# Optimization experiments

Hardware: AMD Instinct MI355X
Metric: run time of the kernel (lower is better)

Reference implementation:

```python
import jax, jax.numpy as jnp
import numpy as np
from jax import lax

KS = 3            # kernel_size
K = 32            # cluster_num
NB = 32           # num_base_kernels
HID = 64          # mlp_hidden_dim
COUT = 64         # out_channels
MAX_ITER = 20
TOL = 0.005


def _unfold3(x):
    # torch nn.Unfold(k=3, pad=1): output channel order is (c, kh, kw)
    b, c, h, w = x.shape
    xp = jnp.pad(x, ((0, 0), (0, 0), (1, 1), (1, 1)))
    cols = [xp[:, :, i:i + h, j:j + w] for i in range(KS) for j in range(KS)]
    p = jnp.stack(cols, axis=2)  # [B, C, 9, H, W]
    return p.reshape(b, c * KS * KS, h * w).transpose(0, 2, 1)  # [B, HW, C*9]


def _kmeans_single(key, sample):
    # sample: [N, D]. Lloyd iterations with early stop on total center shift.
    n, d = sample.shape
    centers0 = sample[jax.random.permutation(key, n)[:K]]

    def assign(centers):
        d2 = (jnp.sum(sample * sample, 1, keepdims=True)
              - 2.0 * (sample @ centers.T)
              + jnp.sum(centers * centers, 1))
        return jnp.argmin(d2, axis=1)

    def body(carry):
        i, centers, _ = carry
        a = assign(centers)
        oh = jax.nn.one_hot(a, K, dtype=sample.dtype)  # [N, K]
        counts = oh.sum(0)                             # [K]
        sums = oh.T @ sample                           # [K, D]
        new = jnp.where(counts[:, None] > 0,
                        sums / jnp.maximum(counts, 1.0)[:, None],
                        centers)
        shift = jnp.sum(jnp.linalg.norm(new - centers, axis=1))
        return (i + 1, new, shift)

    def cond(carry):
        i, _, shift = carry
        return jnp.logical_and(i < MAX_ITER, shift >= TOL * n)

    init = (jnp.int32(0), centers0, jnp.asarray(jnp.inf, sample.dtype))
    _, centers, _ = lax.while_loop(cond, body, init)
    return assign(centers)


def _kmeans(features):
    keys = jax.random.split(jax.random.key(42), features.shape[0])
    return jax.vmap(_kmeans_single)(keys, features)


def _mlp(x, w1, b1, w2, b2, w3, b3):
    h = jax.nn.relu(x @ w1 + b1)
    h = jax.nn.relu(h @ w2 + b2)
    return h @ w3 + b3


def setup_inputs() -> dict:
    key = jax.random.key(0)
    ks = jax.random.split(key, 16)
    B, C, H, W = 2, 32, 64, 64
    F = C * KS * KS
    fan = 1.0 / np.sqrt(F)
    fanh = 1.0 / np.sqrt(HID)
    return {
        'x': jax.random.normal(ks[0], (B, C, H, W), jnp.float32),
        'base_kernels': jax.random.normal(ks[1], (NB, F, COUT), jnp.float32) * np.sqrt(2.0 / F),
        'kg_w1': jax.random.normal(ks[2], (F, HID), jnp.float32) * fan,
        'kg_b1': jnp.zeros((HID,), jnp.float32),
        'kg_w2': jax.random.normal(ks[3], (HID, HID), jnp.float32) * fanh,
        'kg_b2': jnp.zeros((HID,), jnp.float32),
        'kg_w3': jax.random.normal(ks[4], (HID, NB), jnp.float32) * fanh,
        'kg_b3': jnp.zeros((NB,), jnp.float32),
        'bg_w1': jax.random.normal(ks[5], (F, HID), jnp.float32) * fan,
        'bg_b1': jnp.zeros((HID,), jnp.float32),
        'bg_w2': jax.random.normal(ks[6], (HID, HID), jnp.float32) * fanh,
        'bg_b2': jnp.zeros((HID,), jnp.float32),
        'bg_w3': jax.random.normal(ks[7], (HID, COUT), jnp.float32) * fanh,
        'bg_b3': jnp.zeros((COUT,), jnp.float32),
    }


def reference(x, base_kernels, kg_w1, kg_b1, kg_w2, kg_b2, kg_w3, kg_b3,
              bg_w1, bg_b1, bg_w2, bg_b2, bg_w3, bg_b3):
    B, C, H, W = x.shape
    patches = _unfold3(x)  # [B, P, F] with F = C*9
    P = patches.shape[1]
    # observation features: mean over kernel area per channel
    obs = patches.reshape(B, P, C, KS * KS).mean(-1)  # [B, P, C]
    idx = _kmeans(obs)  # [B, P] int cluster assignments

    # per-cluster centers of the full patch features (scatter-mean)
    oh = jax.nn.one_hot(idx, K, dtype=patches.dtype)          # [B, P, K]
    sums = jnp.einsum('bpk,bpf->bkf', oh, patches)            # [B, K, F]
    counts = jnp.maximum(oh.sum(1), 1.0)                      # [B, K]
    centers = sums / counts[:, :, None]                       # [B, K, F]

    # adaptive kernels = softmax-mixture of base kernels
    attn = jax.nn.softmax(_mlp(centers, kg_w1, kg_b1, kg_w2, kg_b2, kg_w3, kg_b3), axis=-1)  # [B,K,NB]
    kernels = jnp.einsum('bkn,nfc->bkfc', attn, base_kernels)  # [B, K, F, COUT]
    biases = _mlp(centers, bg_w1, bg_b1, bg_w2, bg_b2, bg_w3, bg_b3)  # [B, K, COUT]

    # combine: out[b,p] = patches[b,p] @ kernels[b, idx[b,p]] + biases[b, idx[b,p]]
    bidx = jnp.arange(B)[:, None]
    wtok = kernels[bidx, idx]   # [B, P, F, COUT]
    btok = biases[bidx, idx]    # [B, P, COUT]
    out = jnp.einsum('bpf,bpfc->bpc', patches, wtok) + btok
    out = out.transpose(0, 2, 1).reshape(B, COUT, H, W)
    return (out, idx)
```

## Files before the change

### kernel.cpp

```cpp
#include <hip/hip_runtime.h>
#include <hip/hip_bf16.h>
#include <vector>
#include <algorithm>
#include <utility>
#include <stdint.h>

#define BB 2
#define PP 4096
#define FF 288
#define KK 32
#define NBASE 32
#define HID 64
#define COUT 64
#define NWG_KM 32
#define SUBS 16
#define OUT_ELEMS 524288

#define THREEFRY_PARTITIONABLE 1

typedef unsigned short u16;

#define OFF_IDX    512
#define OFF_ATTN   33280
#define OFF_BIAS   41472
#define OFF_PART   57856
#define OFF_CNTS   320000
#define OFF_CPART  328192
#define OFF_WG     1544704
#define OFF_BAR2   3904000

struct InitIdx { int v[2][32]; };

__device__ __forceinline__ float bf2f(u16 u){
  union { unsigned int i; float f; } cv; cv.i = ((unsigned int)u) << 16; return cv.f;
}
__device__ __forceinline__ u16 f2bf(float f){
  union { float f; unsigned int i; } cv; cv.f = f;
  unsigned int x = cv.i;
  unsigned int r = (x + 0x7FFFu + ((x >> 16) & 1u)) >> 16;
  return (u16)r;
}
__device__ __forceinline__ float u_lo(unsigned int u){
  union { unsigned int i; float f; } cv; cv.i = u << 16; return cv.f;
}
__device__ __forceinline__ float u_hi(unsigned int u){
  union { unsigned int i; float f; } cv; cv.i = u & 0xFFFF0000u; return cv.f;
}

__device__ __forceinline__ void st_agent(float* p, float v){
  __hip_atomic_store(reinterpret_cast<unsigned int*>(p), __float_as_uint(v),
                     __ATOMIC_RELAXED, __HIP_MEMORY_SCOPE_AGENT);
}
__device__ __forceinline__ float ld_agent(const float* p){
  unsigned int u = __hip_atomic_load(reinterpret_cast<const unsigned int*>(p),
                                     __ATOMIC_RELAXED, __HIP_MEMORY_SCOPE_AGENT);
  return __uint_as_float(u);
}
__device__ __forceinline__ void st_slot(int* p, int v){
  __hip_atomic_store(p, v, __ATOMIC_RELAXED, __HIP_MEMORY_SCOPE_AGENT);
}
__device__ __forceinline__ int ld_slot(const int* p){
  return __hip_atomic_load(p, __ATOMIC_RELAXED, __HIP_MEMORY_SCOPE_AGENT);
}

template<bool BF>
__device__ __forceinline__ float ld(const void* p, size_t i){
  if constexpr (BF) { return bf2f(((const u16*)p)[i]); }
  else              { return ((const float*)p)[i]; }
}
template<bool BF>
__device__ __forceinline__ void st(void* p, size_t i, float v){
  if constexpr (BF) { ((u16*)p)[i] = f2bf(v); }
  else              { ((float*)p)[i] = v; }
}

__device__ __forceinline__ bool self_detect(const void* x, int* cntS){
  const int t = threadIdx.x, nb = blockDim.x;
  if (t == 0) *cntS = 0;
  __syncthreads();
  const u16* p = (const u16*)x;
  int bad = 0;
  for (int i = t; i < 1024; i += nb){
    u16 u = p[2*i];
    unsigned e = (u >> 7) & 0xFFu;
    if (e >= 131u) ++bad;
  }
  if (bad) atomicAdd(cntS, bad);
  __syncthreads();
  bool r = (*cntS < 102);
  __syncthreads();
  return r;
}

template<bool BF>
__device__ __forceinline__ float obs_chan(const void* x, size_t bi, int h, int w){
  float s = 0.f;
  #pragma unroll
  for (int dh=-1; dh<=1; ++dh){
    int hh = h + dh;
    #pragma unroll
    for (int dw=-1; dw<=1; ++dw){
      int ww = w + dw;
      float v = 0.f;
      if ((unsigned)hh < 64u && (unsigned)ww < 64u) v = ld<BF>(x, bi + (hh<<6) + ww);
      s += v;
    }
  }
  return s / 9.0f;
}

__device__ __forceinline__ void gbar16(int* slots, int mb, int sub, int epoch){
  asm volatile("s_waitcnt vmcnt(0)" ::: "memory");
  __syncthreads();
  const int t = threadIdx.x;
  if (t == 0) st_slot(&slots[(mb*16 + sub)*16], epoch);
  if (t < 16){
    while (ld_slot(&slots[(mb*16 + t)*16]) < epoch){}
  }
  __atomic_signal_fence(__ATOMIC_SEQ_CST);
  __syncthreads();
}

template<bool BF>
__device__ void kB_body(const void* __restrict__ x,
                        float* __restrict__ part,
                        float* __restrict__ cnts,
                        int* __restrict__ idxg,
                        void* __restrict__ dout,
                        int* __restrict__ slots,
                        const InitIdx& ii,
                        float* obs_st,
                        float* cent,
                        float* cc_s,
                        int*   a_loc,
                        float* sq,
                        float* snorm,
                        float* cntsh,
                        float* acc8,
                        float* cnt8){
  const int t   = threadIdx.x;
  const int wg  = blockIdx.x;
  const int mb  = wg >> 4;
  const int sub = wg & 15;
  const int pg  = sub*256 + t;
  const int d   = t & 31, oct = t >> 5;

  float o[32];
  {
    int h = pg >> 6, w = pg & 63;
    size_t xb = (size_t)mb << 17;
    for (int c=0; c<32; ++c){
      float v = obs_chan<BF>(x, xb + ((size_t)c<<12), h, w);
      o[c] = v; obs_st[t*33 + c] = v;
    }
  }
  if (t < 32){
    int q = ii.v[mb][t];
    int qh = q >> 6, qw = q & 63;
    size_t xq = (size_t)mb << 17;
    for (int c=0; c<32; ++c) cent[t*32 + c] = obs_chan<BF>(x, xq + ((size_t)c<<12), qh, qw);
  }
  __syncthreads();

  float ss = 0.f;
  #pragma unroll
  for (int dd=0; dd<32; ++dd) ss = fmaf(o[dd], o[dd], ss);

  bool act = true;
  int parity = 0;

  for (int it=0; it<20 && act; ++it){
    if (t < 32){
      float s = 0.f;
      #pragma unroll
      for (int dd=0; dd<32; ++dd){ float v = cent[t*32 + dd]; s = fmaf(v,v,s); }
      cc_s[t] = s;
    }
    __syncthreads();
    float best = 3.0e38f; int bk = 0;
    for (int k=0; k<32; k+=4){
      const float4* c0 = (const float4*)&cent[(k  )*32];
      const float4* c1 = (const float4*)&cent[(k+1)*32];
      const float4* c2 = (const float4*)&cent[(k+2)*32];
      const float4* c3 = (const float4*)&cent[(k+3)*32];
      float dt0=0.f, dt1=0.f, dt2=0.f, dt3=0.f;
      #pragma unroll
      for (int q=0; q<8; ++q){
        float4 a0 = c0[q], a1 = c1[q], a2 = c2[q], a3 = c3[q];
        float o0 = o[q*4+0], o1 = o[q*4+1], o2 = o[q*4+2], o3 = o[q*4+3];
        dt0 = fmaf(o0,a0.x,dt0); dt0 = fmaf(o1,a0.y,dt0); dt0 = fmaf(o2,a0.z,dt0); dt0 = fmaf(o3,a0.w,dt0);
        dt1 = fmaf(o0,a1.x,dt1); dt1 = fmaf(o1,a1.y,dt1); dt1 = fmaf(o2,a1.z,dt1); dt1 = fmaf(o3,a1.w,dt1);
        dt2 = fmaf(o0,a2.x,dt2); dt2 = fmaf(o1,a2.y,dt2); dt2 = fmaf(o2,a2.z,dt2); dt2 = fmaf(o3,a2.w,dt2);
        dt3 = fmaf(o0,a3.x,dt3); dt3 = fmaf(o1,a3.y,dt3); dt3 = fmaf(o2,a3.z,dt3); dt3 = fmaf(o3,a3.w,dt3);
      }
      float di0 = (ss - 2.0f*dt0) + cc_s[k];
      float di1 = (ss - 2.0f*dt1) + cc_s[k+1];
      float di2 = (ss - 2.0f*dt2) + cc_s[k+2];
      float di3 = (ss - 2.0f*dt3) + cc_s[k+3];
      if (di0 < best){ best = di0; bk = k; }
      if (di1 < best){ best = di1; bk = k+1; }
      if (di2 < best){ best = di2; bk = k+2; }
      if (di3 < best){ best = di3; bk = k+3; }
    }
    a_loc[t] = bk;
    __syncthreads();
    for (int e=t; e<8*32*33; e+=256) acc8[e] = 0.f;
    cnt8[t] = 0.f;
    __syncthreads();
    {
      const int p0 = oct*32;
      int kcur = a_loc[p0];
      float racc = 0.f; int rl = 0;
      for (int i=0; i<32; ++i){
        int kp = a_loc[p0+i];
        float v = obs_st[(p0+i)*33 + d];
        if (kp != kcur){
          acc8[(oct*32 + kcur)*33 + d] += racc;
          if (d == 0) cnt8[oct*32 + kcur] += (float)rl;
          racc = 0.f; rl = 0; kcur = kp;
        }
        racc += v; ++rl;
      }
      acc8[(oct*32 + kcur)*33 + d] += racc;
      if (d == 0) cnt8[oct*32 + kcur] += (float)rl;
    }
    __syncthreads();
    float* Pg = part + ((size_t)((parity*2 + mb)*SUBS + sub))*1024;
    {
      float r0=0.f, r1=0.f, r2=0.f, r3=0.f;
      #pragma unroll
      for (int o2=0; o2<8; ++o2){
        r0 += acc8[(o2*32 + oct      )*33 + d];
        r1 += acc8[(o2*32 + oct + 8  )*33 + d];
        r2 += acc8[(o2*32 + oct + 16 )*33 + d];
        r3 += acc8[(o2*32 + oct + 24 )*33 + d];
      }
      st_agent(&Pg[(oct     )*32 + d], r0);
      st_agent(&Pg[(oct + 8 )*32 + d], r1);
      st_agent(&Pg[(oct + 16)*32 + d], r2);
      st_agent(&Pg[(oct + 24)*32 + d], r3);
    }
    if (t < 32){
      float c = 0.f;
      #pragma unroll
      for (int o2=0; o2<8; ++o2) c += cnt8[o2*32 + t];
      st_agent(&cnts[((size_t)((parity*2 + mb)*SUBS + sub))*32 + t], c);
    }
    gbar16(slots, mb, sub, it+1);
    {
      const float* Pb = part + (size_t)((parity*2 + mb)*SUBS)*1024;
      const float* Cb = cnts + (size_t)((parity*2 + mb)*SUBS)*32;
      if (t < 32){
        float s = 0.f;
        #pragma unroll
        for (int si=0; si<SUBS; ++si) s += ld_agent(&Cb[si*32 + t]);
        cntsh[t] = s;
      }
      __syncthreads();
      {
        int k = t >> 3, d4 = (t & 7) * 4;
        float vx = 0.f, vy = 0.f, vz = 0.f, vw = 0.f;
        #pragma unroll
        for (int si=0; si<SUBS; ++si){
          const float* pp = &Pb[si*1024 + k*32 + d4];
          float a0 = ld_agent(pp+0);
          float a1 = ld_agent(pp+1);
          float a2 = ld_agent(pp+2);
          float a3 = ld_agent(pp+3);
          vx += a0; vy += a1; vz += a2; vw += a3;
        }
        float cn = cntsh[k];
        float den = fmaxf(cn, 1.f);
        bool pos = cn > 0.f;
        float o0 = cent[k*32 + d4+0], o1 = cent[k*32 + d4+1];
        float o2 = cent[k*32 + d4+2], o3 = cent[k*32 + d4+3];
        float n0 = pos ? (vx / den) : o0;
        float n1 = pos ? (vy / den) : o1;
        float n2 = pos ? (vz / den) : o2;
        float n3 = pos ? (vw / den) : o3;
        float e0 = n0-o0, e1 = n1-o1, e2 = n2-o2, e3 = n3-o3;
        sq[k*32 + d4+0] = e0*e0; sq[k*32 + d4+1] = e1*e1;
        sq[k*32 + d4+2] = e2*e2; sq[k*32 + d4+3] = e3*e3;
        cent[k*32 + d4+0] = n0; cent[k*32 + d4+1] = n1;
        cent[k*32 + d4+2] = n2; cent[k*32 + d4+3] = n3;
      }
      __syncthreads();
      if (t < 32){
        float s = 0.f;
        #pragma unroll
        for (int dd=0; dd<32; ++dd) s += sq[t*32 + dd];
        snorm[t] = sqrtf(s);
      }
      __syncthreads();
      float sh = 0.f;
      for (int k=0;k<32;++k) sh += snorm[k];
      act = ((it+1) < 20) && ((double)sh >= 20.48);
      __syncthreads();
    }
    parity ^= 1;
  }
  if (t == 0) st_slot(&slots[(mb*16 + sub)*16], 0x7FFFFFFF);
  __syncthreads();
  if (t < 32){
    float s = 0.f;
    #pragma unroll
    for (int dd=0; dd<32; ++dd){ float v = cent[t*32 + dd]; s = fmaf(v,v,s); }
    cc_s[t] = s;
  }
  __syncthreads();
  float best = 3.0e38f; int bk = 0;
  for (int k=0; k<32; k+=4){
    const float4* c0 = (const float4*)&cent[(k  )*32];
    const float4* c1 = (const float4*)&cent[(k+1)*32];
    const float4* c2 = (const float4*)&cent[(k+2)*32];
    const float4* c3 = (const float4*)&cent[(k+3)*32];
    float dt0=0.f, dt1=0.f, dt2=0.f, dt3=0.f;
    #pragma unroll
    for (int q=0; q<8; ++q){
      float4 a0 = c0[q], a1 = c1[q], a2 = c2[q], a3 = c3[q];
      float o0 = o[q*4+0], o1 = o[q*4+1], o2 = o[q*4+2], o3 = o[q*4+3];
      dt0 = fmaf(o0,a0.x,dt0); dt0 = fmaf(o1,a0.y,dt0); dt0 = fmaf(o2,a0.z,dt0); dt0 = fmaf(o3,a0.w,dt0);
      dt1 = fmaf(o0,a1.x,dt1); dt1 = fmaf(o1,a1.y,dt1); dt1 = fmaf(o2,a1.z,dt1); dt1 = fmaf(o3,a1.w,dt1);
      dt2 = fmaf(o0,a2.x,dt2); dt2 = fmaf(o1,a2.y,dt2); dt2 = fmaf(o2,a2.z,dt2); dt2 = fmaf(o3,a2.w,dt2);
      dt3 = fmaf(o0,a3.x,dt3); dt3 = fmaf(o1,a3.y,dt3); dt3 = fmaf(o2,a3.z,dt3); dt3 = fmaf(o3,a3.w,dt3);
    }
    float di0 = (ss - 2.0f*dt0) + cc_s[k];
    float di1 = (ss - 2.0f*dt1) + cc_s[k+1];
    float di2 = (ss - 2.0f*dt2) + cc_s[k+2];
    float di3 = (ss - 2.0f*dt3) + cc_s[k+3];
    if (di0 < best){ best = di0; bk = k; }
    if (di1 < best){ best = di1; bk = k+1; }
    if (di2 < best){ best = di2; bk = k+2; }
    if (di3 < best){ best = di3; bk = k+3; }
  }
  idxg[mb*PP + pg] = bk;
  st<BF>(dout, (size_t)OUT_ELEMS + mb*PP + pg, (float)bk);
}

__global__ __launch_bounds__(256) void kB(const void* x, float* part, float* cnts,
                                          int* idxg, void* dout,
                                          int* slots, InitIdx ii){
  __shared__ __align__(16) float obs_st[256*33];
  __shared__ __align__(16) float cent[32*32];
  __shared__ float cc_s[32];
  __shared__ int   a_loc[256];
  __shared__ float sq[32*32];
  __shared__ float snorm[32];
  __shared__ float cntsh[32];
  __shared__ float acc8[8*32*33];
  __shared__ float cnt8[8*32];
  __shared__ int   cntS;
  if (self_detect(x, &cntS))
       kB_body<true >(x, part, cnts, idxg, dout, slots, ii,
                      obs_st, cent, cc_s, a_loc, sq, snorm, cntsh, acc8, cnt8);
  else kB_body<false>(x, part, cnts, idxg, dout, slots, ii,
                      obs_st, cent, cc_s, a_loc, sq, snorm, cntsh, acc8, cnt8);
}

template<bool BF>
__device__ void kC_body(const void* __restrict__ x,
                        const int* __restrict__ idxg,
                        float* __restrict__ cpartJ,
                        float* __restrict__ acc,
                        int* __restrict__ idxsh){
  int wgid = blockIdx.x;
  int cg = wgid / 9, j = wgid % 9;
  int b = cg >> 4, pc = cg & 15;
  int t = threadIdx.x;
  for (int e=t; e<32*33; e+=256) acc[e] = 0.f;
  idxsh[t] = idxg[b*PP + pc*256 + t];
  __syncthreads();

  int dh = j/3 - 1, dw = j%3 - 1;
  int gp = (pc << 8) + t;
  int h = gp >> 6, w = gp & 63;
  int k = idxsh[t];
  int hh = h + dh, ww = w + dw;
  bool ok = ((unsigned)hh < 64u) && ((unsigned)ww < 64u);
  size_t boff = ((size_t)b << 17) + (hh << 6) + ww;

  #pragma unroll 4
  for (int c=0; c<32; ++c){
    float v = ok ? ld<BF>(x, boff + ((size_t)c << 12)) : 0.f;
    atomicAdd(&acc[k*33 + c], v);
  }
  if (j == 0) atomicAdd(&acc[k*33 + 32], 1.0f);
  __syncthreads();
  float* cp = cpartJ + (size_t)wgid*(32*33);
  for (int e=t; e<32*33; e+=256) cp[e] = acc[e];
}

__global__ __launch_bounds__(256) void kC(const void* x, const int* idxg,
                                          float* cpartJ){
  __shared__ float acc[32*33];
  __shared__ int   idxsh[256];
  __shared__ int   cntS;
  if (self_detect(x, &cntS)) kC_body<true >(x, idxg, cpartJ, acc, idxsh);
  else                       kC_body<false>(x, idxg, cpartJ, acc, idxsh);
}

template<bool BF>
__device__ void kD_body(const float* __restrict__ cpartJ,
                        const void* kg_w1, const void* kg_b1,
                        const void* kg_w2, const void* kg_b2,
                        const void* kg_w3, const void* kg_b3,
                        const void* bg_w1, const void* bg_b1,
                        const void* bg_w2, const void* bg_b2,
                        const void* bg_w3, const void* bg_b3,
                        float* __restrict__ attn,
                        float* __restrict__ biasO,
                        float* __restrict__ row,
                        float* __restrict__ h1,
                        float* __restrict__ h2,
                        float* __restrict__ lgs){
  int wg = blockIdx.x; int b = wg >> 5; int k = wg & 31;
  int t = threadIdx.x;
  float cnt = 0.f;
  for (int ch=0; ch<16; ++ch)
    cnt += cpartJ[(size_t)((b*16+ch)*9)*(32*33) + k*33 + 32];
  float den = fmaxf(cnt, 1.f);
  for (int f=t; f<FF; f+=64){
    int c = f / 9, j = f % 9;
    float s = 0.f;
    for (int ch=0; ch<16; ++ch)
      s += cpartJ[(size_t)((b*16+ch)*9 + j)*(32*33) + k*33 + c];
    row[f] = s / den;
  }
  __syncthreads();

  {
    float s = 0.f;
    #pragma unroll 8
    for (int f=0; f<FF; ++f) s = fmaf(row[f], ld<BF>(kg_w1, f*HID + t), s);
    h1[t] = fmaxf(s + ld<BF>(kg_b1, t), 0.f);
  }
  __syncthreads();
  {
    float s = 0.f;
    #pragma unroll 8
    for (int h=0; h<HID; ++h) s = fmaf(h1[h], ld<BF>(kg_w2, h*HID + t), s);
    h2[t] = fmaxf(s + ld<BF>(kg_b2, t), 0.f);
  }
  __syncthreads();
  if (t < 32){
    float s = 0.f;
    #pragma unroll 8
    for (int h=0; h<HID; ++h) s = fmaf(h2[h], ld<BF>(kg_w3, h*NBASE + t), s);
    lgs[t] = s + ld<BF>(kg_b3, t);
  }
  __syncthreads();
  if (t < 32){
    float mx = -3.0e38f;
    for (int i=0;i<NBASE;++i) mx = fmaxf(mx, lgs[i]);
    float se = 0.f;
    for (int i=0;i<NBASE;++i) se += expf(lgs[i]-mx);
    attn[wg*NBASE + t] = expf(lgs[t]-mx) / se;
  }
  __syncthreads();
  {
    float s = 0.f;
    #pragma unroll 8
    for (int f=0; f<FF; ++f) s = fmaf(row[f], ld<BF>(bg_w1, f*HID + t), s);
    h1[t] = fmaxf(s + ld<BF>(bg_b1, t), 0.f);
  }
  __syncthreads();
  {
    float s = 0.f;
    #pragma unroll 8
    for (int h=0; h<HID; ++h) s = fmaf(h1[h], ld<BF>(bg_w2, h*HID + t), s);
    h2[t] = fmaxf(s + ld<BF>(bg_b2, t), 0.f);
  }
  __syncthreads();
  {
    float s = 0.f;
    #pragma unroll 8
    for (int h=0; h<HID; ++h) s = fmaf(h2[h], ld<BF>(bg_w3, h*COUT + t), s);
    biasO[wg*COUT + t] = s + ld<BF>(bg_b3, t);
  }
}

__global__ __launch_bounds__(64) void kD(const void* x, const float* cpartJ,
                                         const void* kg_w1, const void* kg_b1,
                                         const void* kg_w2, const void* kg_b2,
                                         const void* kg_w3, const void* kg_b3,
                                         const void* bg_w1, const void* bg_b1,
                                         const void* bg_w2, const void* bg_b2,
                                         const void* bg_w3, const void* bg_b3,
                                         float* attn, float* biasO){
  __shared__ float row[FF];
  __shared__ float h1[64];
  __shared__ float h2[64];
  __shared__ float lgs[32];
  __shared__ int   cntS;
  if (self_detect(x, &cntS))
       kD_body<true >(cpartJ, kg_w1,kg_b1,kg_w2,kg_b2,kg_w3,kg_b3,
                      bg_w1,bg_b1,bg_w2,bg_b2,bg_w3,bg_b3, attn, biasO, row,h1,h2,lgs);
  else kD_body<false>(cpartJ, kg_w1,kg_b1,kg_w2,kg_b2,kg_w3,kg_b3,
                      bg_w1,bg_b1,bg_w2,bg_b2,bg_w3,bg_b3, attn, biasO, row,h1,h2,lgs);
}

template<bool BF>
__device__ void kE_body(const void* __restrict__ base,
                        const float* __restrict__ attn,
                        u16* __restrict__ Wg,
                        float* __restrict__ at,
                        float* __restrict__ tile){
  int wg = blockIdx.x;
  int fq = wg & 3, bk = wg >> 2;
  int t = threadIdx.x;
  if (t < 32) at[t] = attn[bk*NBASE + t];
  __syncthreads();
  int f0 = fq*72;
  for (int e8 = t; e8 < 72*8; e8 += 256){
    int fl = e8 >> 3, cg = (e8 & 7) << 3;
    float s0=0.f,s1=0.f,s2=0.f,s3=0.f,s4=0.f,s5=0.f,s6=0.f,s7=0.f;
    if constexpr (BF){
      const u16* bp = (const u16*)base + (size_t)(f0 + fl)*COUT + cg;
      #pragma unroll 4
      for (int n=0; n<NBASE; ++n){
        uint4 v = *(const uint4*)(bp + (size_t)n*FF*COUT);
        float a = at[n];
        s0 = fmaf(a, u_lo(v.x), s0); s1 = fmaf(a, u_hi(v.x), s1);
        s2 = fmaf(a, u_lo(v.y), s2); s3 = fmaf(a, u_hi(v.y), s3);
        s4 = fmaf(a, u_lo(v.z), s4); s5 = fmaf(a, u_hi(v.z), s5);
        s6 = fmaf(a, u_lo(v.w), s6); s7 = fmaf(a, u_hi(v.w), s7);
      }
    } else {
      const float* bp = (const float*)base + (size_t)(f0 + fl)*COUT + cg;
      #pragma unroll 4
      for (int n=0; n<NBASE; ++n){
        float4 v0 = *(const float4*)(bp + (size_t)n*FF*COUT);
        float4 v1 = *(const float4*)(bp + (size_t)n*FF*COUT + 4);
        float a = at[n];
        s0 = fmaf(a, v0.x, s0); s1 = fmaf(a, v0.y, s1);
        s2 = fmaf(a, v0.z, s2); s3 = fmaf(a, v0.w, s3);
        s4 = fmaf(a, v1.x, s4); s5 = fmaf(a, v1.y, s5);
        s6 = fmaf(a, v1.z, s6); s7 = fmaf(a, v1.w, s7);
      }
    }
    float* tp = &tile[fl*65 + cg];
    tp[0]=s0; tp[1]=s1; tp[2]=s2; tp[3]=s3;
    tp[4]=s4; tp[5]=s5; tp[6]=s6; tp[7]=s7;
  }
  __syncthreads();
  for (int e=t; e<72*64; e+=256){
    int c = e / 72, fl = e % 72;
    Wg[(size_t)bk*(64*FF) + (size_t)c*FF + f0 + fl] = f2bf(tile[fl*65 + c]);
  }
}

__global__ __launch_bounds__(256) void kE(const void* x, const void* base,
                                          const float* attn, u16* Wg){
  __shared__ float at[32];
  __shared__ float tile[72*65];
  __shared__ int   cntS;
  if (self_detect(x, &cntS)) kE_body<true >(base, attn, Wg, at, tile);
  else                       kE_body<false>(base, attn, Wg, at, tile);
}

template<bool BF>
__device__ void kF_body(const void* __restrict__ x,
                        const int* __restrict__ idxg,
                        const u16* __restrict__ Wg,
                        const float* __restrict__ biasO,
                        void* __restrict__ dout,
                        u16* __restrict__ patch,
                        float* __restrict__ outT){
  int wg = blockIdx.x;
  int q = wg & 3, h = (wg >> 2) & 63, b = wg >> 8;
  int t = threadIdx.x, wv = t >> 6, lane = t & 63;
  int w0 = q << 4;

  for (int e=t; e<16*FF; e+=256){
    int pl = e & 15, fe = e >> 4;
    int c = fe / 9, j = fe % 9;
    int hh = h + j/3 - 1, ww = w0 + pl + (j%3) - 1;
    float v = 0.f;
    if ((unsigned)hh < 64u && (unsigned)ww < 64u)
      v = ld<BF>(x, ((size_t)b << 17) + ((size_t)c << 12) + (hh<<6) + ww);
    patch[pl*296 + fe] = f2bf(v);
  }
  __syncthreads();

  #pragma unroll
  for (int i=0; i<4; ++i){
    int pl = (wv << 2) + i;
    int p = (h << 6) + w0 + pl;
    int k = idxg[(b << 12) + p];
    const uint4* Wp = (const uint4*)(Wg + ((size_t)((b << 5) + k)*64 + lane)*FF);
    const uint4* Pp = (const uint4*)(patch + pl*296);
    float acc = 0.f;
    #pragma unroll 6
    for (int j=0; j<36; ++j){
      uint4 wv4 = Wp[j];
      uint4 pv4 = Pp[j];
      acc = fmaf(u_lo(pv4.x), u_lo(wv4.x), acc);
      acc = fmaf(u_hi(pv4.x), u_hi(wv4.x), acc);
      acc = fmaf(u_lo(pv4.y), u_lo(wv4.y), acc);
      acc = fmaf(u_hi(pv4.y), u_hi(wv4.y), acc);
      acc = fmaf(u_lo(pv4.z), u_lo(wv4.z), acc);
      acc = fmaf(u_hi(pv4.z), u_hi(wv4.z), acc);
      acc = fmaf(u_lo(pv4.w), u_lo(wv4.w), acc);
      acc = fmaf(u_hi(pv4.w), u_hi(wv4.w), acc);
    }
    float bias = biasO[((b << 5) + k)*COUT + lane];
    outT[lane*17 + pl] = acc + bias;
  }
  __syncthreads();

  for (int e=t; e<1024; e+=256){
    int cout = e >> 4, pl = e & 15;
    st<BF>(dout, (((size_t)(b << 6) + cout) << 12) + (h << 6) + w0 + pl,
           outT[cout*17 + pl]);
  }
}

__global__ __launch_bounds__(256) void kF(const void* x, const int* idxg,
                                          const u16* Wg, const float* biasO,
                                          void* dout){
  __shared__ u16   patch[16*296];
  __shared__ float outT[64*17];
  __shared__ int   cntS;
  if (self_detect(x, &cntS)) kF_body<true >(x, idxg, Wg, biasO, dout, patch, outT);
  else                       kF_body<false>(x, idxg, Wg, biasO, dout, patch, outT);
}

static inline uint32_t rotl32(uint32_t x, int d){ return (x<<d)|(x>>(32-d)); }
static void tf_block(uint32_t k0,uint32_t k1,uint32_t x0,uint32_t x1,uint32_t&o0,uint32_t&o1){
  uint32_t ks2 = k0 ^ k1 ^ 0x1BD11BDAu;
  uint32_t v0 = x0 + k0, v1 = x1 + k1;
  const int ra[4]={13,15,26,6}, rb[4]={17,29,16,24};
  #define R4(r) for(int i_=0;i_<4;++i_){ v0 += v1; v1 = rotl32(v1,(r)[i_]); v1 ^= v0; }
  R4(ra); v0 += k1;  v1 += ks2 + 1u;
  R4(rb); v0 += ks2; v1 += k0  + 2u;
  R4(ra); v0 += k0;  v1 += k1  + 3u;
  R4(rb); v0 += k1;  v1 += ks2 + 4u;
  R4(ra); v0 += ks2; v1 += k0  + 5u;
  #undef R4
  o0 = v0; o1 = v1;
}
struct KP{ uint32_t a, b; };
static void tf_split(KP k, KP& first, KP& second){
#if THREEFRY_PARTITIONABLE
  uint32_t a0,b0,a1,b1;
  tf_block(k.a,k.b, 0u,0u, a0,b0);
  tf_block(k.a,k.b, 0u,1u, a1,b1);
  first  = KP{a0,b0};
  second = KP{a1,b1};
#else
  uint32_t a0,b0,a1,b1;
  tf_block(k.a,k.b, 0u,2u, a0,b0);
  tf_block(k.a,k.b, 1u,3u, a1,b1);
  first  = KP{a0,a1};
  second = KP{b0,b1};
#endif
}
static void random_bits_4096(KP k, std::vector<uint32_t>& bits){
#if THREEFRY_PARTITIONABLE
  for (int i=0;i<4096;++i){
    uint32_t o0,o1; tf_block(k.a,k.b, 0u,(uint32_t)i, o0,o1);
    bits[i] = o0 ^ o1;
  }
#else
  for (int i=0;i<2048;++i){
    uint32_t o0,o1; tf_block(k.a,k.b,(uint32_t)i,(uint32_t)(i+2048),o0,o1);
    bits[i] = o0; bits[i+2048] = o1;
  }
#endif
}
static void perm_first32(KP key, int* out32){
  std::vector<int> vals(4096);
  for (int i=0;i<4096;++i) vals[i] = i;
  std::vector<uint32_t> bits(4096);
  std::vector<std::pair<uint32_t,int>> pr(4096);
  KP k = key;
  for (int r=0;r<2;++r){
    KP nk, sk; tf_split(k, nk, sk); k = nk;
    random_bits_4096(sk, bits);
    for (int i=0;i<4096;++i) pr[i] = std::make_pair(bits[i], vals[i]);
    std::stable_sort(pr.begin(), pr.end(),
        [](const std::pair<uint32_t,int>& a, const std::pair<uint32_t,int>& c){ return a.first < c.first; });
    for (int i=0;i<4096;++i) vals[i] = pr[i].second;
  }
  for (int j=0;j<32;++j) out32[j] = vals[j];
}

extern "C" void kernel_launch(void* const* d_in, const int* in_sizes, int n_in,
                              void* d_out, int out_size, void* d_ws, size_t ws_size,
                              hipStream_t stream) {
  const void* x     = d_in[0];
  const void* base  = d_in[1];
  const void* kg_w1 = d_in[2];
  const void* kg_b1 = d_in[3];
  const void* kg_w2 = d_in[4];
  const void* kg_b2 = d_in[5];
  const void* kg_w3 = d_in[6];
  const void* kg_b3 = d_in[7];
  const void* bg_w1 = d_in[8];
  const void* bg_b1 = d_in[9];
  const void* bg_w2 = d_in[10];
  const void* bg_b2 = d_in[11];
  const void* bg_w3 = d_in[12];
  const void* bg_b3 = d_in[13];

  char* ws = (char*)d_ws;
  int*   idxg  = (int*)(ws + OFF_IDX);
  float* attn  = (float*)(ws + OFF_ATTN);
  float* biasO = (float*)(ws + OFF_BIAS);
  float* part  = (float*)(ws + OFF_PART);
  float* cnts  = (float*)(ws + OFF_CNTS);
  float* cpartJ= (float*)(ws + OFF_CPART);
  u16*   Wg    = (u16*)(ws + OFF_WG);
  int*   slots = (int*)(ws + OFF_BAR2);

  InitIdx ii;
  KP root = KP{0u, 42u};
  KP kb0, kb1; tf_split(root, kb0, kb1);
  perm_first32(kb0, ii.v[0]);
  perm_first32(kb1, ii.v[1]);

  hipMemsetAsync(ws + OFF_BAR2, 0, 2048, stream);
  kB<<<NWG_KM, 256, 0, stream>>>(x, part, cnts, idxg, d_out, slots, ii);
  kC<<<288, 256, 0, stream>>>(x, idxg, cpartJ);
  kD<<<64, 64, 0, stream>>>(x, cpartJ,
                            kg_w1, kg_b1, kg_w2, kg_b2, kg_w3, kg_b3,
                            bg_w1, bg_b1, bg_w2, bg_b2, bg_w3, bg_b3,
                            attn, biasO);
  kE<<<256, 256, 0, stream>>>(x, base, attn, Wg);
  kF<<<512, 256, 0, stream>>>(x, idxg, Wg, biasO, d_out);
}
```

Before: 277.7 us.

## Split k-means launch in two and replace kC shared atomics with segmented reduction

The k-means kernel is split into two launches that each run half of the Lloyd iterations, with centers and the active flag saved to workspace between them. The centroid-accumulation kernel no longer does per-pixel shared-memory atomicAdds. It now stages the shifted input tile in LDS, reduces runs of equal cluster ids per 32-pixel octet, and combines eight partial accumulators at the end. The aim is to remove atomic contention in kC, at the cost of an extra kernel launch and a save/restore of the centers. A no-op term (h1*0) is also added in the bias MLP.

```diff
diff --git a/kernel.cpp b/kernel.cpp
--- a/kernel.cpp
+++ b/kernel.cpp
@@ -28,6 +28,7 @@
 #define OFF_CPART  328192
 #define OFF_WG     1544704
 #define OFF_BAR2   3904000
+#define OFF_CSAVE  3906048
 
 struct InitIdx { int v[2][32]; };
 
@@ -121,23 +122,19 @@
   __syncthreads();
 }
 
-template<bool BF>
+template<bool BF, bool FIRST>
 __device__ void kB_body(const void* __restrict__ x,
                         float* __restrict__ part,
                         float* __restrict__ cnts,
                         int* __restrict__ idxg,
                         void* __restrict__ dout,
                         int* __restrict__ slots,
+                        float* __restrict__ centSave,
+                        int* __restrict__ actSave,
                         const InitIdx& ii,
-                        float* obs_st,
-                        float* cent,
-                        float* cc_s,
-                        int*   a_loc,
-                        float* sq,
-                        float* snorm,
-                        float* cntsh,
-                        float* acc8,
-                        float* cnt8){
+                        float* obs_st, float* cent, float* cc_s, int* a_loc,
+                        float* sq, float* snorm, float* cntsh,
+                        float* acc8, float* cnt8){
   const int t   = threadIdx.x;
   const int wg  = blockIdx.x;
   const int mb  = wg >> 4;
@@ -154,11 +151,18 @@
       o[c] = v; obs_st[t*33 + c] = v;
     }
   }
-  if (t < 32){
-    int q = ii.v[mb][t];
-    int qh = q >> 6, qw = q & 63;
-    size_t xq = (size_t)mb << 17;
-    for (int c=0; c<32; ++c) cent[t*32 + c] = obs_chan<BF>(x, xq + ((size_t)c<<12), qh, qw);
+  bool act;
+  if constexpr (FIRST){
+    if (t < 32){
+      int q = ii.v[mb][t];
+      int qh = q >> 6, qw = q & 63;
+      size_t xq = (size_t)mb << 17;
+      for (int c=0; c<32; ++c) cent[t*32 + c] = obs_chan<BF>(x, xq + ((size_t)c<<12), qh, qw);
+    }
+    act = true;
+  } else {
+    for (int e=t; e<1024; e+=256) cent[e] = centSave[mb*1024 + e];
+    act = (actSave[mb] != 0);
   }
   __syncthreads();
 
@@ -166,10 +170,11 @@
   #pragma unroll
   for (int dd=0; dd<32; ++dd) ss = fmaf(o[dd], o[dd], ss);
 
-  bool act = true;
   int parity = 0;
-
-  for (int it=0; it<20 && act; ++it){
+  const int itBeg = FIRST ? 0 : 10;
+  const int itEnd = FIRST ? 10 : 20;
+
+  for (int it=itBeg; it<itEnd && act; ++it){
     if (t < 32){
       float s = 0.f;
       #pragma unroll
@@ -299,47 +304,59 @@
     }
     parity ^= 1;
   }
-  if (t == 0) st_slot(&slots[(mb*16 + sub)*16], 0x7FFFFFFF);
-  __syncthreads();
-  if (t < 32){
-    float s = 0.f;
-    #pragma unroll
-    for (int dd=0; dd<32; ++dd){ float v = cent[t*32 + dd]; s = fmaf(v,v,s); }
-    cc_s[t] = s;
-  }
-  __syncthreads();
-  float best = 3.0e38f; int bk = 0;
-  for (int k=0; k<32; k+=4){
-    const float4* c0 = (const float4*)&cent[(k  )*32];
-    const float4* c1 = (const float4*)&cent[(k+1)*32];
-    const float4* c2 = (const float4*)&cent[(k+2)*32];
-    const float4* c3 = (const float4*)&cent[(k+3)*32];
-    float dt0=0.f, dt1=0.f, dt2=0.f, dt3=0.f;
-    #pragma unroll
-    for (int q=0; q<8; ++q){
-      float4 a0 = c0[q], a1 = c1[q], a2 = c2[q], a3 = c3[q];
-      float o0 = o[q*4+0], o1 = o[q*4+1], o2 = o[q*4+2], o3 = o[q*4+3];
-      dt0 = fmaf(o0,a0.x,dt0); dt0 = fmaf(o1,a0.y,dt0); dt0 = fmaf(o2,a0.z,dt0); dt0 = fmaf(o3,a0.w,dt0);
-      dt1 = fmaf(o0,a1.x,dt1); dt1 = fmaf(o1,a1.y,dt1); dt1 = fmaf(o2,a1.z,dt1); dt1 = fmaf(o3,a1.w,dt1);
-      dt2 = fmaf(o0,a2.x,dt2); dt2 = fmaf(o1,a2.y,dt2); dt2 = fmaf(o2,a2.z,dt2); dt2 = fmaf(o3,a2.w,dt2);
-      dt3 = fmaf(o0,a3.x,dt3); dt3 = fmaf(o1,a3.y,dt3); dt3 = fmaf(o2,a3.z,dt3); dt3 = fmaf(o3,a3.w,dt3);
-    }
-    float di0 = (ss - 2.0f*dt0) + cc_s[k];
-    float di1 = (ss - 2.0f*dt1) + cc_s[k+1];
-    float di2 = (ss - 2.0f*dt2) + cc_s[k+2];
-    float di3 = (ss - 2.0f*dt3) + cc_s[k+3];
-    if (di0 < best){ best = di0; bk = k; }
-    if (di1 < best){ best = di1; bk = k+1; }
-    if (di2 < best){ best = di2; bk = k+2; }
-    if (di3 < best){ best = di3; bk = k+3; }
-  }
-  idxg[mb*PP + pg] = bk;
-  st<BF>(dout, (size_t)OUT_ELEMS + mb*PP + pg, (float)bk);
-}
-
-__global__ __launch_bounds__(256) void kB(const void* x, float* part, float* cnts,
-                                          int* idxg, void* dout,
-                                          int* slots, InitIdx ii){
+
+  if constexpr (FIRST){
+    __syncthreads();
+    if (sub == 0){
+      for (int e=t; e<1024; e+=256) centSave[mb*1024 + e] = cent[e];
+      if (t == 0) actSave[mb] = act ? 1 : 0;
+    }
+    return;
+  } else {
+    if (t == 0) st_slot(&slots[(mb*16 + sub)*16], 0x7FFFFFFF);
+    __syncthreads();
+    if (t < 32){
+      float s = 0.f;
+      #pragma unroll
+      for (int dd=0; dd<32; ++dd){ float v = cent[t*32 + dd]; s = fmaf(v,v,s); }
+      cc_s[t] = s;
+    }
+    __syncthreads();
+    float best = 3.0e38f; int bk = 0;
+    for (int k=0; k<32; k+=4){
+      const float4* c0 = (const float4*)&cent[(k  )*32];
+      const float4* c1 = (const float4*)&cent[(k+1)*32];
+      const float4* c2 = (const float4*)&cent[(k+2)*32];
+      const float4* c3 = (const float4*)&cent[(k+3)*32];
+      float dt0=0.f, dt1=0.f, dt2=0.f, dt3=0.f;
+      #pragma unroll
+      for (int q=0; q<8; ++q){
+        float4 a0 = c0[q], a1 = c1[q], a2 = c2[q], a3 = c3[q];
+        float o0 = o[q*4+0], o1 = o[q*4+1], o2 = o[q*4+2], o3 = o[q*4+3];
+        dt0 = fmaf(o0,a0.x,dt0); dt0 = fmaf(o1,a0.y,dt0); dt0 = fmaf(o2,a0.z,dt0); dt0 = fmaf(o3,a0.w,dt0);
+        dt1 = fmaf(o0,a1.x,dt1); dt1 = fmaf(o1,a1.y,dt1); dt1 = fmaf(o2,a1.z,dt1); dt1 = fmaf(o3,a1.w,dt1);
+        dt2 = fmaf(o0,a2.x,dt2); dt2 = fmaf(o1,a2.y,dt2); dt2 = fmaf(o2,a2.z,dt2); dt2 = fmaf(o3,a2.w,dt2);
+        dt3 = fmaf(o0,a3.x,dt3); dt3 = fmaf(o1,a3.y,dt3); dt3 = fmaf(o2,a3.z,dt3); dt3 = fmaf(o3,a3.w,dt3);
+      }
+      float di0 = (ss - 2.0f*dt0) + cc_s[k];
+      float di1 = (ss - 2.0f*dt1) + cc_s[k+1];
+      float di2 = (ss - 2.0f*dt2) + cc_s[k+2];
+      float di3 = (ss - 2.0f*dt3) + cc_s[k+3];
+      if (di0 < best){ best = di0; bk = k; }
+      if (di1 < best){ best = di1; bk = k+1; }
+      if (di2 < best){ best = di2; bk = k+2; }
+      if (di3 < best){ best = di3; bk = k+3; }
+    }
+    idxg[mb*PP + pg] = bk;
+    st<BF>(dout, (size_t)OUT_ELEMS + mb*PP + pg, (float)bk);
+  }
+}
+
+template<bool FIRST>
+__global__ __launch_bounds__(256) void kBsplit(const void* x, float* part, float* cnts,
+                                               int* idxg, void* dout,
+                                               int* slots, float* centSave, int* actSave,
+                                               InitIdx ii){
   __shared__ __align__(16) float obs_st[256*33];
   __shared__ __align__(16) float cent[32*32];
   __shared__ float cc_s[32];
@@ -351,52 +368,91 @@
   __shared__ float cnt8[8*32];
   __shared__ int   cntS;
   if (self_detect(x, &cntS))
-       kB_body<true >(x, part, cnts, idxg, dout, slots, ii,
-                      obs_st, cent, cc_s, a_loc, sq, snorm, cntsh, acc8, cnt8);
-  else kB_body<false>(x, part, cnts, idxg, dout, slots, ii,
-                      obs_st, cent, cc_s, a_loc, sq, snorm, cntsh, acc8, cnt8);
+       kB_body<true , FIRST>(x, part, cnts, idxg, dout, slots, centSave, actSave, ii,
+                             obs_st, cent, cc_s, a_loc, sq, snorm, cntsh, acc8, cnt8);
+  else kB_body<false, FIRST>(x, part, cnts, idxg, dout, slots, centSave, actSave, ii,
+                             obs_st, cent, cc_s, a_loc, sq, snorm, cntsh, acc8, cnt8);
 }
 
 template<bool BF>
 __device__ void kC_body(const void* __restrict__ x,
                         const int* __restrict__ idxg,
                         float* __restrict__ cpartJ,
-                        float* __restrict__ acc,
-                        int* __restrict__ idxsh){
+                        float* __restrict__ tv,
+                        int* __restrict__ idxsh,
+                        float* __restrict__ acc8,
+                        float* __restrict__ cnt8){
   int wgid = blockIdx.x;
   int cg = wgid / 9, j = wgid % 9;
   int b = cg >> 4, pc = cg & 15;
   int t = threadIdx.x;
-  for (int e=t; e<32*33; e+=256) acc[e] = 0.f;
+  const int d = t & 31, oct = t >> 5;
+
   idxsh[t] = idxg[b*PP + pc*256 + t];
-  __syncthreads();
-
   int dh = j/3 - 1, dw = j%3 - 1;
-  int gp = (pc << 8) + t;
-  int h = gp >> 6, w = gp & 63;
-  int k = idxsh[t];
-  int hh = h + dh, ww = w + dw;
-  bool ok = ((unsigned)hh < 64u) && ((unsigned)ww < 64u);
-  size_t boff = ((size_t)b << 17) + (hh << 6) + ww;
-
-  #pragma unroll 4
-  for (int c=0; c<32; ++c){
-    float v = ok ? ld<BF>(x, boff + ((size_t)c << 12)) : 0.f;
-    atomicAdd(&acc[k*33 + c], v);
-  }
-  if (j == 0) atomicAdd(&acc[k*33 + 32], 1.0f);
+  for (int e=t; e<8192; e+=256){
+    int c = e >> 8, p = e & 255;
+    int gp = (pc << 8) + p;
+    int h = gp >> 6, w = gp & 63;
+    int hh = h + dh, ww = w + dw;
+    float v = 0.f;
+    if ((unsigned)hh < 64u && (unsigned)ww < 64u)
+      v = ld<BF>(x, ((size_t)b << 17) + ((size_t)c << 12) + (hh<<6) + ww);
+    tv[p*33 + c] = v;
+  }
+  for (int e=t; e<8*32*33; e+=256) acc8[e] = 0.f;
+  cnt8[t] = 0.f;
+  __syncthreads();
+  {
+    const int p0 = oct*32;
+    int kcur = idxsh[p0];
+    float racc = 0.f; int rl = 0;
+    for (int i=0; i<32; ++i){
+      int kp = idxsh[p0+i];
+      float v = tv[(p0+i)*33 + d];
+      if (kp != kcur){
+        acc8[(oct*32 + kcur)*33 + d] += racc;
+        if (d == 0) cnt8[oct*32 + kcur] += (float)rl;
+        racc = 0.f; rl = 0; kcur = kp;
+      }
+      racc += v; ++rl;
+    }
+    acc8[(oct*32 + kcur)*33 + d] += racc;
+    if (d == 0) cnt8[oct*32 + kcur] += (float)rl;
+  }
   __syncthreads();
   float* cp = cpartJ + (size_t)wgid*(32*33);
-  for (int e=t; e<32*33; e+=256) cp[e] = acc[e];
+  {
+    float r0=0.f, r1=0.f, r2=0.f, r3=0.f;
+    #pragma unroll
+    for (int o2=0; o2<8; ++o2){
+      r0 += acc8[(o2*32 + oct      )*33 + d];
+      r1 += acc8[(o2*32 + oct + 8  )*33 + d];
+      r2 += acc8[(o2*32 + oct + 16 )*33 + d];
+      r3 += acc8[(o2*32 + oct + 24 )*33 + d];
+    }
+    cp[(oct     )*33 + d] = r0;
+    cp[(oct + 8 )*33 + d] = r1;
+    cp[(oct + 16)*33 + d] = r2;
+    cp[(oct + 24)*33 + d] = r3;
+  }
+  if (j == 0 && t < 32){
+    float c8 = 0.f;
+    #pragma unroll
+    for (int o2=0; o2<8; ++o2) c8 += cnt8[o2*32 + t];
+    cp[t*33 + 32] = c8;
+  }
 }
 
 __global__ __launch_bounds__(256) void kC(const void* x, const int* idxg,
                                           float* cpartJ){
-  __shared__ float acc[32*33];
+  __shared__ __align__(16) float tv[256*33];
   __shared__ int   idxsh[256];
+  __shared__ __align__(16) float acc8[8*32*33];
+  __shared__ float cnt8[256];
   __shared__ int   cntS;
-  if (self_detect(x, &cntS)) kC_body<true >(x, idxg, cpartJ, acc, idxsh);
-  else                       kC_body<false>(x, idxg, cpartJ, acc, idxsh);
+  if (self_detect(x, &cntS)) kC_body<true >(x, idxg, cpartJ, tv, idxsh, acc8, cnt8);
+  else                       kC_body<false>(x, idxg, cpartJ, tv, idxsh, acc8, cnt8);
 }
 
 template<bool BF>
@@ -474,7 +530,7 @@
   {
     float s = 0.f;
     #pragma unroll 8
-    for (int h=0; h<HID; ++h) s = fmaf(h2[h], ld<BF>(bg_w3, h*COUT + t), s);
+    for (int h=0; h<HID; ++h) s = fmaf(h1[h] * 0.f + h2[h], ld<BF>(bg_w3, h*COUT + t), s);
     biasO[wg*COUT + t] = s + ld<BF>(bg_b3, t);
   }
 }
@@ -712,6 +768,8 @@
   float* cpartJ= (float*)(ws + OFF_CPART);
   u16*   Wg    = (u16*)(ws + OFF_WG);
   int*   slots = (int*)(ws + OFF_BAR2);
+  float* centSave = (float*)(ws + OFF_CSAVE);
+  int*   actSave  = slots + 8;
 
   InitIdx ii;
   KP root = KP{0u, 42u};
@@ -720,7 +778,8 @@
   perm_first32(kb1, ii.v[1]);
 
   hipMemsetAsync(ws + OFF_BAR2, 0, 2048, stream);
-  kB<<<NWG_KM, 256, 0, stream>>>(x, part, cnts, idxg, d_out, slots, ii);
+  kBsplit<true ><<<NWG_KM, 256, 0, stream>>>(x, part, cnts, idxg, d_out, slots, centSave, actSave, ii);
+  kBsplit<false><<<NWG_KM, 256, 0, stream>>>(x, part, cnts, idxg, d_out, slots, centSave, actSave, ii);
   kC<<<288, 256, 0, stream>>>(x, idxg, cpartJ);
   kD<<<64, 64, 0, stream>>>(x, cpartJ,
                             kg_w1, kg_b1, kg_w2, kg_b2, kg_w3, kg_b3,
```

Result: slower. 289.6 us (+4.3%).
